# Kernel optimization log

Measured on AMD Instinct MI355X. Metric: run time of the kernel, lower is better.

The kernel has to match this reference:

```python
import jax, jax.numpy as jnp
import numpy as np

PATCH = 14          # config.patch_size
MAX_SEQ = 2048      # config.max_vit_seq_len
A2 = 4              # adaptor_patch_size ** 2
GRID = 32           # max_image_size // patch_size -> sqrt(num_positions - 1)
EPS = 1e-5          # layer_norm_eps

IMG_SIZES = [(448, 448), (448, 672), (336, 336), (224, 448), (560, 560), (336, 448)]


def bilinear_resize_chw(img, oh, ow):
    # torch F.interpolate(mode='bilinear', align_corners=False): half-pixel centers, edge clamp
    C, H, W = img.shape
    def coords(o, i):
        c = (jnp.arange(o, dtype=jnp.float32) + 0.5) * (i / o) - 0.5
        c = jnp.clip(c, 0.0, i - 1.0)
        lo = jnp.floor(c).astype(jnp.int32)
        hi = jnp.minimum(lo + 1, i - 1)
        return lo, hi, c - lo
    y0, y1, wy = coords(oh, H)
    x0, x1, wx = coords(ow, W)
    top = img[:, y0][:, :, x0] * (1 - wx) + img[:, y0][:, :, x1] * wx
    bot = img[:, y1][:, :, x0] * (1 - wx) + img[:, y1][:, :, x1] * wx
    wy = wy[None, :, None]
    return top * (1 - wy) + bot * wy


def patch_embed(img, conv_w, conv_b):
    # Conv2d(k=stride=PATCH) == non-overlapping patch extract + matmul
    C, H, W = img.shape
    h, w = H // PATCH, W // PATCH
    x = img[:, :h * PATCH, :w * PATCH].reshape(C, h, PATCH, w, PATCH)
    x = x.transpose(1, 3, 0, 2, 4).reshape(h * w, C * PATCH * PATCH)  # [hw, c*kh*kw]
    out = x @ conv_w.reshape(conv_w.shape[0], -1).T + conv_b          # [hw, E]
    return out, (h, w)


def pos_embed_interp(pos_table, h, w):
    pe = pos_table[1:]  # drop cls position, [GRID*GRID, E]
    if (h, w) == (GRID, GRID):
        return pe
    E = pe.shape[-1]
    pe2d = pe.reshape(GRID, GRID, E).transpose(2, 0, 1)  # [E, GRID, GRID]
    pe2d = bilinear_resize_chw(pe2d, h, w)
    return pe2d.transpose(1, 2, 0).reshape(h * w, E)


def layernorm(x, g, b):
    m = x.mean(-1, keepdims=True)
    v = ((x - m) ** 2).mean(-1, keepdims=True)
    return (x - m) / jnp.sqrt(v + EPS) * g + b


def pack_positions(hw_list):
    # static replay of group_images_by_max_seq_len + a2 rescale in forward
    pos, batch_idx, seq_len = [], 0, 0
    for (h, w) in hw_list:
        L = h * w
        if seq_len + L > MAX_SEQ:
            batch_idx += 1
            seq_len = 0
        s = (seq_len // A2) * A2
        pos.append((batch_idx, s, s + (L // A2) * A2))
        seq_len += L
    return pos, batch_idx + 1


def setup_inputs() -> dict:
    key = jax.random.key(0)
    ks = jax.random.split(key, 9)
    E = 1280
    inp = {}
    for i, (H, W) in enumerate(IMG_SIZES):
        inp[f'img{i}'] = jax.random.normal(ks[i], (3, H, W), dtype=jnp.float32)
    inp['conv_w'] = jax.random.normal(ks[6], (E, 3, PATCH, PATCH), dtype=jnp.float32) * 0.02
    inp['conv_b'] = jnp.zeros((E,), dtype=jnp.float32)
    inp['pos_table'] = jax.random.normal(ks[7], (GRID * GRID + 1, E), dtype=jnp.float32) * 0.02
    inp['ln_w'] = jnp.ones((E,), dtype=jnp.float32)
    inp['ln_b'] = jnp.zeros((E,), dtype=jnp.float32)
    return inp


def reference(img0, img1, img2, img3, img4, img5, conv_w, conv_b, pos_table, ln_w, ln_b):
    images = [img0, img1, img2, img3, img4, img5]
    E = conv_w.shape[0]
    hw = [(im.shape[1] // PATCH, im.shape[2] // PATCH) for im in images]
    positions, B = pack_positions(hw)
    emb = jnp.zeros((B, MAX_SEQ, E), dtype=jnp.float32)
    mask = np.zeros((B, 1, MAX_SEQ, MAX_SEQ), dtype=bool)
    for im, (bi, s, e) in zip(images, positions):
        x, (h, w) = patch_embed(im, conv_w, conv_b)
        x = x + pos_embed_interp(pos_table, h, w)
        x = layernorm(x, ln_w, ln_b)
        emb = emb.at[bi, s:e].set(x)
        mask[bi, 0, s:e, s:e] = True
    return emb, jnp.asarray(mask)
```

## Files before the change

kernel.cpp:

```cpp
#include <hip/hip_runtime.h>
#include <hip/hip_bf16.h>
#include <stdint.h>

#define E_DIM 1280
#define KDIM 588
#define KPAD 608
#define M_TOTAL 6016
#define EMB_FLOATS (5*2048*1280)
#define MASK_FLOATS (5*2048*2048)

typedef __attribute__((ext_vector_type(8))) short bf16x8;
typedef __attribute__((ext_vector_type(4))) float f32x4;

__device__ __forceinline__ unsigned short f2bf(float f) {
    unsigned int u = __float_as_uint(f);
    u += 0x7fff + ((u >> 16) & 1);
    return (unsigned short)(u >> 16);
}

__global__ __launch_bounds__(256) void extract_patches(
    const float* __restrict__ i0, const float* __restrict__ i1,
    const float* __restrict__ i2, const float* __restrict__ i3,
    const float* __restrict__ i4, const float* __restrict__ i5,
    unsigned short* __restrict__ A)
{
    int idx = blockIdx.x * 256 + threadIdx.x;
    if (idx >= M_TOTAL * KPAD) return;
    int r = idx / KPAD;
    int k = idx - r * KPAD;
    unsigned short v = 0;
    if (k < KDIM) {
        const int rowOff[7] = {0,1024,2560,3136,3648,5248,6016};
        const int wA[6]     = {32,48,24,32,40,32};
        const int WA[6]     = {448,672,336,448,560,448};
        const int planeA[6] = {200704,301056,112896,100352,313600,150528};
        const float* imgs[6] = {i0,i1,i2,i3,i4,i5};
        int img = 0;
        #pragma unroll
        for (int i = 1; i < 6; ++i) if (r >= rowOff[i]) img = i;
        int ri = r - rowOff[img];
        int w = wA[img], W = WA[img], plane = planeA[img];
        int py = ri / w, px = ri - py * w;
        int c  = k / 196;
        int rem = k - c * 196;
        int iy = rem / 14, ix = rem - iy * 14;
        float pix = imgs[img][(size_t)c * plane + (size_t)(py*14 + iy) * W + (px*14 + ix)];
        v = f2bf(pix);
    }
    A[idx] = v;
}

__global__ __launch_bounds__(256) void convert_w(
    const float* __restrict__ cw, unsigned short* __restrict__ Wb)
{
    int idx = blockIdx.x * 256 + threadIdx.x;
    if (idx >= E_DIM * KPAD) return;
    int e = idx / KPAD;
    int k = idx - e * KPAD;
    Wb[idx] = (k < KDIM) ? f2bf(cw[(size_t)e * KDIM + k]) : (unsigned short)0;
}

__global__ __launch_bounds__(256) void gemm_bf16(
    const unsigned short* __restrict__ A,
    const unsigned short* __restrict__ Bm,
    float* __restrict__ C)
{
    __shared__ __align__(16) unsigned short As[128*32];
    __shared__ __align__(16) unsigned short Bs[128*32];
    const int t  = threadIdx.x;
    const int m0 = blockIdx.x * 128;
    const int n0 = blockIdx.y * 128;
    const int lane = t & 63;
    const int wv = t >> 6;
    const int wr = wv >> 1, wc = wv & 1;
    const int l16 = lane & 15, q = lane >> 4;

    f32x4 acc[4][4] = {};

    for (int kk = 0; kk < KPAD; kk += 32) {
        #pragma unroll
        for (int i = 0; i < 2; ++i) {
            int off = i * 4096 + t * 16;
            int row = off >> 6;
            int kb  = (off & 63) >> 1;
            const unsigned short* ga = A  + (size_t)(m0 + row) * KPAD + kk + kb;
            __builtin_amdgcn_global_load_lds(
                (const __attribute__((address_space(1))) void*)ga,
                (__attribute__((address_space(3))) void*)((char*)As + off), 16, 0, 0);
            const unsigned short* gb = Bm + (size_t)(n0 + row) * KPAD + kk + kb;
            __builtin_amdgcn_global_load_lds(
                (const __attribute__((address_space(1))) void*)gb,
                (__attribute__((address_space(3))) void*)((char*)Bs + off), 16, 0, 0);
        }
        __syncthreads();

        bf16x8 af[4], bfr[4];
        #pragma unroll
        for (int mi = 0; mi < 4; ++mi)
            af[mi] = *(const bf16x8*)&As[(wr*64 + mi*16 + l16) * 32 + q * 8];
        #pragma unroll
        for (int ni = 0; ni < 4; ++ni)
            bfr[ni] = *(const bf16x8*)&Bs[(wc*64 + ni*16 + l16) * 32 + q * 8];
        #pragma unroll
        for (int mi = 0; mi < 4; ++mi)
            #pragma unroll
            for (int ni = 0; ni < 4; ++ni)
                acc[mi][ni] = __builtin_amdgcn_mfma_f32_16x16x32_bf16(
                    af[mi], bfr[ni], acc[mi][ni], 0, 0, 0);
        __syncthreads();
    }

    #pragma unroll
    for (int mi = 0; mi < 4; ++mi) {
        #pragma unroll
        for (int ni = 0; ni < 4; ++ni) {
            int col = n0 + wc*64 + ni*16 + l16;
            #pragma unroll
            for (int reg = 0; reg < 4; ++reg) {
                int rowr = m0 + wr*64 + mi*16 + q*4 + reg;
                C[(size_t)rowr * E_DIM + col] = acc[mi][ni][reg];
            }
        }
    }
}

__global__ __launch_bounds__(256) void epilogue(
    const float* __restrict__ C, const float* __restrict__ pos_table,
    const float* __restrict__ conv_b,
    const float* __restrict__ ln_w, const float* __restrict__ ln_b,
    float* __restrict__ out)
{
    const int r = blockIdx.x;
    const int t = threadIdx.x;
    const int rowOff[7]  = {0,1024,2560,3136,3648,5248,6016};
    const int hA[6]      = {32,32,24,16,40,24};
    const int wA[6]      = {32,48,24,32,40,32};
    const int outBase[6] = {0, 2048, 4096, 4672, 6144, 8192};

    int img = 0;
    #pragma unroll
    for (int i = 1; i < 6; ++i) if (r >= rowOff[i]) img = i;
    int ri = r - rowOff[img];
    int h = hA[img], w = wA[img];
    int y = ri / w, x = ri - y * w;

    float cy = fminf(fmaxf((y + 0.5f) * (32.0f / h) - 0.5f, 0.0f), 31.0f);
    float cx = fminf(fmaxf((x + 0.5f) * (32.0f / w) - 0.5f, 0.0f), 31.0f);
    int y0 = (int)floorf(cy); int y1 = min(y0 + 1, 31); float wy = cy - (float)y0;
    int x0 = (int)floorf(cx); int x1 = min(x0 + 1, 31); float wx = cx - (float)x0;

    const float* P00 = pos_table + (size_t)(1 + y0*32 + x0) * E_DIM;
    const float* P01 = pos_table + (size_t)(1 + y0*32 + x1) * E_DIM;
    const float* P10 = pos_table + (size_t)(1 + y1*32 + x0) * E_DIM;
    const float* P11 = pos_table + (size_t)(1 + y1*32 + x1) * E_DIM;

    float vals[5];
    float s = 0.f, s2 = 0.f;
    #pragma unroll
    for (int j = 0; j < 5; ++j) {
        int e = t + j * 256;
        float p = (1.f - wy) * ((1.f - wx) * P00[e] + wx * P01[e])
                +        wy  * ((1.f - wx) * P10[e] + wx * P11[e]);
        float v = C[(size_t)r * E_DIM + e] + conv_b[e] + p;
        vals[j] = v;
        s += v; s2 += v * v;
    }
    #pragma unroll
    for (int o = 32; o > 0; o >>= 1) {
        s  += __shfl_down(s,  o, 64);
        s2 += __shfl_down(s2, o, 64);
    }
    __shared__ float ls[8];
    int lane = t & 63, wvi = t >> 6;
    if (lane == 0) { ls[wvi] = s; ls[4 + wvi] = s2; }
    __syncthreads();
    if (t == 0) {
        float ts  = ls[0] + ls[1] + ls[2] + ls[3];
        float ts2 = ls[4] + ls[5] + ls[6] + ls[7];
        float m   = ts / 1280.f;
        float var = ts2 / 1280.f - m * m;
        ls[0] = m;
        ls[1] = 1.f / sqrtf(var + 1e-5f);
    }
    __syncthreads();
    float m = ls[0], inv = ls[1];
    size_t ob = (size_t)(outBase[img] + ri) * E_DIM;
    #pragma unroll
    for (int j = 0; j < 5; ++j) {
        int e = t + j * 256;
        out[ob + e] = (vals[j] - m) * inv * ln_w[e] + ln_b[e];
    }
}

__global__ __launch_bounds__(256) void fill_rest(float4* __restrict__ out4)
{
    const int TOT4 = (EMB_FLOATS + MASK_FLOATS) / 4;
    int idx = blockIdx.x * 256 + threadIdx.x;
    if (idx >= TOT4) return;
    size_t flat = (size_t)idx * 4;
    if (flat < (size_t)EMB_FLOATS) {
        int row = (int)(flat / E_DIM);
        int b   = row >> 11;
        int seq = row & 2047;
        const int filled[5] = {1024,1536,1088,1600,768};
        if (seq >= filled[b]) {
            out4[idx] = make_float4(0.f, 0.f, 0.f, 0.f);
        }
    } else {
        size_t mrem = flat - (size_t)EMB_FLOATS;
        int b  = (int)(mrem >> 22);
        int rr = (int)(mrem >> 11) & 2047;
        int c0 = (int)(mrem & 2047);
        const int h0[5] = {1024,1536,576,1600,768};
        const int l1[5] = {0,0,576,0,0};
        const int h1[5] = {0,0,1088,0,0};
        bool rin0 = rr < h0[b];
        bool rin1 = (rr >= l1[b]) && (rr < h1[b]) && (h1[b] > 0);
        float4 v;
        float* vp = &v.x;
        #pragma unroll
        for (int j = 0; j < 4; ++j) {
            int c = c0 + j;
            bool on = (rin0 && c < h0[b]) ||
                      (rin1 && c >= l1[b] && c < h1[b]);
            vp[j] = on ? 1.f : 0.f;
        }
        out4[idx] = v;
    }
}

extern "C" void kernel_launch(void* const* d_in, const int* in_sizes, int n_in,
                              void* d_out, int out_size, void* d_ws, size_t ws_size,
                              hipStream_t stream) {
    const float* img0 = (const float*)d_in[0];
    const float* img1 = (const float*)d_in[1];
    const float* img2 = (const float*)d_in[2];
    const float* img3 = (const float*)d_in[3];
    const float* img4 = (const float*)d_in[4];
    const float* img5 = (const float*)d_in[5];
    const float* conv_w    = (const float*)d_in[6];
    const float* conv_b    = (const float*)d_in[7];
    const float* pos_table = (const float*)d_in[8];
    const float* ln_w      = (const float*)d_in[9];
    const float* ln_b      = (const float*)d_in[10];
    float* out = (float*)d_out;

    unsigned short* Abf = (unsigned short*)d_ws;
    unsigned short* Wbf = Abf + (size_t)M_TOTAL * KPAD;
    float* Cbuf = out + EMB_FLOATS;

    int nA = M_TOTAL * KPAD;
    extract_patches<<<(nA + 255) / 256, 256, 0, stream>>>(
        img0, img1, img2, img3, img4, img5, Abf);

    int nW = E_DIM * KPAD;
    convert_w<<<(nW + 255) / 256, 256, 0, stream>>>(conv_w, Wbf);

    dim3 g(M_TOTAL / 128, E_DIM / 128);
    gemm_bf16<<<g, 256, 0, stream>>>(Abf, Wbf, Cbuf);

    epilogue<<<M_TOTAL, 256, 0, stream>>>(Cbuf, pos_table, conv_b, ln_w, ln_b, out);

    int tot4 = (EMB_FLOATS + MASK_FLOATS) / 4;
    fill_rest<<<(tot4 + 255) / 256, 256, 0, stream>>>((float4*)out);
}
```

Before: 219.6 us.

## Fuse prep, weight convert, and fill into one launch; vectorize epilogue

Merges patch extraction, weight bf16 conversion, padding-row zeroing and mask filling into a single kernel. Each image gets its own block range with template-constant dimensions, and only the unfilled embedding rows are zeroed. The GEMM output buffer moves from the mask region to workspace, so mask writes no longer have to wait until after the epilogue. The epilogue uses 320 threads each handling one float4, which cuts per-row memory instructions at the cost of assuming the workspace is large enough for the extra C buffer.

```diff
diff --git a/kernel.cpp b/kernel.cpp
--- a/kernel.cpp
+++ b/kernel.cpp
@@ -9,6 +9,12 @@
 #define EMB_FLOATS (5*2048*1280)
 #define MASK_FLOATS (5*2048*2048)
 
+#define EXT_BLOCKS  14288
+#define CW_BLOCKS   3040
+#define ZERO_BLOCKS 5280
+#define MASK_BLOCKS 20480
+#define TOTAL_BLOCKS (EXT_BLOCKS + CW_BLOCKS + ZERO_BLOCKS + MASK_BLOCKS)
+
 typedef __attribute__((ext_vector_type(8))) short bf16x8;
 typedef __attribute__((ext_vector_type(4))) float f32x4;
 
@@ -18,46 +24,82 @@
     return (unsigned short)(u >> 16);
 }
 
-__global__ __launch_bounds__(256) void extract_patches(
+template<int PW, int IMGW, int PLANE>
+__device__ __forceinline__ void do_extract(const float* __restrict__ img,
+                                           unsigned short* __restrict__ A,
+                                           int flatBase, int local)
+{
+    int r_local = local / KPAD;
+    int k = local - r_local * KPAD;
+    unsigned short v = 0;
+    if (k < KDIM) {
+        int py = r_local / PW;  int px = r_local - py * PW;
+        int c  = k / 196;       int rem = k - c * 196;
+        int iy = rem / 14;      int ix = rem - iy * 14;
+        v = f2bf(img[(size_t)c * PLANE + (size_t)(py*14 + iy) * IMGW + (px*14 + ix)]);
+    }
+    A[flatBase + local] = v;
+}
+
+__global__ __launch_bounds__(256) void fused_prep(
     const float* __restrict__ i0, const float* __restrict__ i1,
     const float* __restrict__ i2, const float* __restrict__ i3,
     const float* __restrict__ i4, const float* __restrict__ i5,
-    unsigned short* __restrict__ A)
-{
-    int idx = blockIdx.x * 256 + threadIdx.x;
-    if (idx >= M_TOTAL * KPAD) return;
-    int r = idx / KPAD;
-    int k = idx - r * KPAD;
-    unsigned short v = 0;
-    if (k < KDIM) {
-        const int rowOff[7] = {0,1024,2560,3136,3648,5248,6016};
-        const int wA[6]     = {32,48,24,32,40,32};
-        const int WA[6]     = {448,672,336,448,560,448};
-        const int planeA[6] = {200704,301056,112896,100352,313600,150528};
-        const float* imgs[6] = {i0,i1,i2,i3,i4,i5};
-        int img = 0;
-        #pragma unroll
-        for (int i = 1; i < 6; ++i) if (r >= rowOff[i]) img = i;
-        int ri = r - rowOff[img];
-        int w = wA[img], W = WA[img], plane = planeA[img];
-        int py = ri / w, px = ri - py * w;
-        int c  = k / 196;
-        int rem = k - c * 196;
-        int iy = rem / 14, ix = rem - iy * 14;
-        float pix = imgs[img][(size_t)c * plane + (size_t)(py*14 + iy) * W + (px*14 + ix)];
-        v = f2bf(pix);
-    }
-    A[idx] = v;
-}
-
-__global__ __launch_bounds__(256) void convert_w(
-    const float* __restrict__ cw, unsigned short* __restrict__ Wb)
-{
-    int idx = blockIdx.x * 256 + threadIdx.x;
-    if (idx >= E_DIM * KPAD) return;
-    int e = idx / KPAD;
-    int k = idx - e * KPAD;
-    Wb[idx] = (k < KDIM) ? f2bf(cw[(size_t)e * KDIM + k]) : (unsigned short)0;
+    const float* __restrict__ conv_w,
+    unsigned short* __restrict__ A, unsigned short* __restrict__ Wb,
+    float4* __restrict__ out4)
+{
+    const int bid = blockIdx.x;
+    const int t = threadIdx.x;
+
+    if (bid < EXT_BLOCKS) {
+        if (bid < 2432) {
+            int local = bid * 256 + t;
+            do_extract<32,448,200704>(i0, A, 0, local);
+        } else if (bid < 6080) {
+            int local = (bid - 2432) * 256 + t;
+            do_extract<48,672,301056>(i1, A, 2432*256, local);
+        } else if (bid < 7448) {
+            int local = (bid - 6080) * 256 + t;
+            do_extract<24,336,112896>(i2, A, 6080*256, local);
+        } else if (bid < 8664) {
+            int local = (bid - 7448) * 256 + t;
+            do_extract<32,448,100352>(i3, A, 7448*256, local);
+        } else if (bid < 12464) {
+            int local = (bid - 8664) * 256 + t;
+            do_extract<40,560,313600>(i4, A, 8664*256, local);
+        } else {
+            int local = (bid - 12464) * 256 + t;
+            do_extract<32,448,150528>(i5, A, 12464*256, local);
+        }
+    } else if (bid < EXT_BLOCKS + CW_BLOCKS) {
+        int idx = (bid - EXT_BLOCKS) * 256 + t;
+        int e = idx / KPAD;
+        int k = idx - e * KPAD;
+        Wb[idx] = (k < KDIM) ? f2bf(conv_w[(size_t)e * KDIM + k]) : (unsigned short)0;
+    } else if (bid < EXT_BLOCKS + CW_BLOCKS + ZERO_BLOCKS) {
+        int idx = (bid - EXT_BLOCKS - CW_BLOCKS) * 256 + t;
+        int zrow = idx / 320;
+        int c4   = idx - zrow * 320;
+        int b, rowInB;
+        if      (zrow < 1024) { b = 0; rowInB = 1024 + zrow; }
+        else if (zrow < 1536) { b = 1; rowInB = 1536 + (zrow - 1024); }
+        else if (zrow < 2496) { b = 2; rowInB = 1088 + (zrow - 1536); }
+        else if (zrow < 2944) { b = 3; rowInB = 1600 + (zrow - 2496); }
+        else                  { b = 4; rowInB =  768 + (zrow - 2944); }
+        size_t o4 = ((size_t)(b * 2048 + rowInB) * E_DIM) / 4 + c4;
+        out4[o4] = make_float4(0.f, 0.f, 0.f, 0.f);
+    } else {
+        int m4 = (bid - EXT_BLOCKS - CW_BLOCKS - ZERO_BLOCKS) * 256 + t;
+        int b  = m4 >> 20;
+        int rr = (m4 >> 9) & 2047;
+        int c0 = (m4 & 511) * 4;
+        int h0 = (b == 0) ? 1024 : (b == 1) ? 1536 : (b == 2) ? 576 : (b == 3) ? 1600 : 768;
+        bool on = (rr < h0 && c0 < h0);
+        if (b == 2) on = on || (rr >= 576 && rr < 1088 && c0 >= 576 && c0 < 1088);
+        float f = on ? 1.f : 0.f;
+        out4[(size_t)(EMB_FLOATS / 4) + m4] = make_float4(f, f, f, f);
+    }
 }
 
 __global__ __launch_bounds__(256) void gemm_bf16(
@@ -124,7 +166,7 @@
     }
 }
 
-__global__ __launch_bounds__(256) void epilogue(
+__global__ __launch_bounds__(320) void epilogue(
     const float* __restrict__ C, const float* __restrict__ pos_table,
     const float* __restrict__ conv_b,
     const float* __restrict__ ln_w, const float* __restrict__ ln_b,
@@ -132,16 +174,14 @@
 {
     const int r = blockIdx.x;
     const int t = threadIdx.x;
-    const int rowOff[7]  = {0,1024,2560,3136,3648,5248,6016};
-    const int hA[6]      = {32,32,24,16,40,24};
-    const int wA[6]      = {32,48,24,32,40,32};
-    const int outBase[6] = {0, 2048, 4096, 4672, 6144, 8192};
-
-    int img = 0;
-    #pragma unroll
-    for (int i = 1; i < 6; ++i) if (r >= rowOff[i]) img = i;
-    int ri = r - rowOff[img];
-    int h = hA[img], w = wA[img];
+
+    int img     = (r < 1024) ? 0 : (r < 2560) ? 1 : (r < 3136) ? 2 : (r < 3648) ? 3 : (r < 5248) ? 4 : 5;
+    int rowOff  = (img == 0) ? 0 : (img == 1) ? 1024 : (img == 2) ? 2560 : (img == 3) ? 3136 : (img == 4) ? 3648 : 5248;
+    int h       = (img == 0) ? 32 : (img == 1) ? 32 : (img == 2) ? 24 : (img == 3) ? 16 : (img == 4) ? 40 : 24;
+    int w       = (img == 0) ? 32 : (img == 1) ? 48 : (img == 2) ? 24 : (img == 3) ? 32 : (img == 4) ? 40 : 32;
+    int outBase = (img == 0) ? 0 : (img == 1) ? 2048 : (img == 2) ? 4096 : (img == 3) ? 4672 : (img == 4) ? 6144 : 8192;
+
+    int ri = r - rowOff;
     int y = ri / w, x = ri - y * w;
 
     float cy = fminf(fmaxf((y + 0.5f) * (32.0f / h) - 0.5f, 0.0f), 31.0f);
@@ -149,34 +189,38 @@
     int y0 = (int)floorf(cy); int y1 = min(y0 + 1, 31); float wy = cy - (float)y0;
     int x0 = (int)floorf(cx); int x1 = min(x0 + 1, 31); float wx = cx - (float)x0;
 
-    const float* P00 = pos_table + (size_t)(1 + y0*32 + x0) * E_DIM;
-    const float* P01 = pos_table + (size_t)(1 + y0*32 + x1) * E_DIM;
-    const float* P10 = pos_table + (size_t)(1 + y1*32 + x0) * E_DIM;
-    const float* P11 = pos_table + (size_t)(1 + y1*32 + x1) * E_DIM;
-
-    float vals[5];
-    float s = 0.f, s2 = 0.f;
-    #pragma unroll
-    for (int j = 0; j < 5; ++j) {
-        int e = t + j * 256;
-        float p = (1.f - wy) * ((1.f - wx) * P00[e] + wx * P01[e])
-                +        wy  * ((1.f - wx) * P10[e] + wx * P11[e]);
-        float v = C[(size_t)r * E_DIM + e] + conv_b[e] + p;
-        vals[j] = v;
-        s += v; s2 += v * v;
-    }
+    const float4* P00 = (const float4*)(pos_table + (size_t)(1 + y0*32 + x0) * E_DIM);
+    const float4* P01 = (const float4*)(pos_table + (size_t)(1 + y0*32 + x1) * E_DIM);
+    const float4* P10 = (const float4*)(pos_table + (size_t)(1 + y1*32 + x0) * E_DIM);
+    const float4* P11 = (const float4*)(pos_table + (size_t)(1 + y1*32 + x1) * E_DIM);
+    const float4* C4  = (const float4*)(C + (size_t)r * E_DIM);
+    const float4* B4  = (const float4*)conv_b;
+
+    float w00 = (1.f - wy) * (1.f - wx), w01 = (1.f - wy) * wx;
+    float w10 = wy * (1.f - wx),         w11 = wy * wx;
+
+    float4 a = P00[t], b2 = P01[t], c2 = P10[t], d2 = P11[t];
+    float4 cv = C4[t], bv = B4[t];
+    float4 v;
+    v.x = cv.x + bv.x + w00*a.x + w01*b2.x + w10*c2.x + w11*d2.x;
+    v.y = cv.y + bv.y + w00*a.y + w01*b2.y + w10*c2.y + w11*d2.y;
+    v.z = cv.z + bv.z + w00*a.z + w01*b2.z + w10*c2.z + w11*d2.z;
+    v.w = cv.w + bv.w + w00*a.w + w01*b2.w + w10*c2.w + w11*d2.w;
+
+    float s  = v.x + v.y + v.z + v.w;
+    float s2 = v.x*v.x + v.y*v.y + v.z*v.z + v.w*v.w;
     #pragma unroll
     for (int o = 32; o > 0; o >>= 1) {
         s  += __shfl_down(s,  o, 64);
         s2 += __shfl_down(s2, o, 64);
     }
-    __shared__ float ls[8];
+    __shared__ float ls[12];
     int lane = t & 63, wvi = t >> 6;
-    if (lane == 0) { ls[wvi] = s; ls[4 + wvi] = s2; }
+    if (lane == 0) { ls[wvi] = s; ls[6 + wvi] = s2; }
     __syncthreads();
     if (t == 0) {
-        float ts  = ls[0] + ls[1] + ls[2] + ls[3];
-        float ts2 = ls[4] + ls[5] + ls[6] + ls[7];
+        float ts  = ls[0] + ls[1] + ls[2] + ls[3] + ls[4];
+        float ts2 = ls[6] + ls[7] + ls[8] + ls[9] + ls[10];
         float m   = ts / 1280.f;
         float var = ts2 / 1280.f - m * m;
         ls[0] = m;
@@ -184,49 +228,14 @@
     }
     __syncthreads();
     float m = ls[0], inv = ls[1];
-    size_t ob = (size_t)(outBase[img] + ri) * E_DIM;
-    #pragma unroll
-    for (int j = 0; j < 5; ++j) {
-        int e = t + j * 256;
-        out[ob + e] = (vals[j] - m) * inv * ln_w[e] + ln_b[e];
-    }
-}
-
-__global__ __launch_bounds__(256) void fill_rest(float4* __restrict__ out4)
-{
-    const int TOT4 = (EMB_FLOATS + MASK_FLOATS) / 4;
-    int idx = blockIdx.x * 256 + threadIdx.x;
-    if (idx >= TOT4) return;
-    size_t flat = (size_t)idx * 4;
-    if (flat < (size_t)EMB_FLOATS) {
-        int row = (int)(flat / E_DIM);
-        int b   = row >> 11;
-        int seq = row & 2047;
-        const int filled[5] = {1024,1536,1088,1600,768};
-        if (seq >= filled[b]) {
-            out4[idx] = make_float4(0.f, 0.f, 0.f, 0.f);
-        }
-    } else {
-        size_t mrem = flat - (size_t)EMB_FLOATS;
-        int b  = (int)(mrem >> 22);
-        int rr = (int)(mrem >> 11) & 2047;
-        int c0 = (int)(mrem & 2047);
-        const int h0[5] = {1024,1536,576,1600,768};
-        const int l1[5] = {0,0,576,0,0};
-        const int h1[5] = {0,0,1088,0,0};
-        bool rin0 = rr < h0[b];
-        bool rin1 = (rr >= l1[b]) && (rr < h1[b]) && (h1[b] > 0);
-        float4 v;
-        float* vp = &v.x;
-        #pragma unroll
-        for (int j = 0; j < 4; ++j) {
-            int c = c0 + j;
-            bool on = (rin0 && c < h0[b]) ||
-                      (rin1 && c >= l1[b] && c < h1[b]);
-            vp[j] = on ? 1.f : 0.f;
-        }
-        out4[idx] = v;
-    }
+
+    float4 g = ((const float4*)ln_w)[t], be = ((const float4*)ln_b)[t];
+    float4 o4;
+    o4.x = (v.x - m) * inv * g.x + be.x;
+    o4.y = (v.y - m) * inv * g.y + be.y;
+    o4.z = (v.z - m) * inv * g.z + be.z;
+    o4.w = (v.w - m) * inv * g.w + be.w;
+    ((float4*)(out + (size_t)(outBase + ri) * E_DIM))[t] = o4;
 }
 
 extern "C" void kernel_launch(void* const* d_in, const int* in_sizes, int n_in,
@@ -247,20 +256,13 @@
 
     unsigned short* Abf = (unsigned short*)d_ws;
     unsigned short* Wbf = Abf + (size_t)M_TOTAL * KPAD;
-    float* Cbuf = out + EMB_FLOATS;
-
-    int nA = M_TOTAL * KPAD;
-    extract_patches<<<(nA + 255) / 256, 256, 0, stream>>>(
-        img0, img1, img2, img3, img4, img5, Abf);
-
-    int nW = E_DIM * KPAD;
-    convert_w<<<(nW + 255) / 256, 256, 0, stream>>>(conv_w, Wbf);
+    float* Cbuf = (float*)(Wbf + (size_t)E_DIM * KPAD);
+
+    fused_prep<<<TOTAL_BLOCKS, 256, 0, stream>>>(
+        img0, img1, img2, img3, img4, img5, conv_w, Abf, Wbf, (float4*)out);
 
     dim3 g(M_TOTAL / 128, E_DIM / 128);
     gemm_bf16<<<g, 256, 0, stream>>>(Abf, Wbf, Cbuf);
 
-    epilogue<<<M_TOTAL, 256, 0, stream>>>(Cbuf, pos_table, conv_b, ln_w, ln_b, out);
-
-    int tot4 = (EMB_FLOATS + MASK_FLOATS) / 4;
-    fill_rest<<<(tot4 + 255) / 256, 256, 0, stream>>>((float4*)out);
-}
+    epilogue<<<M_TOTAL, 320, 0, stream>>>(Cbuf, pos_table, conv_b, ln_w, ln_b, out);
+}
```

Result: faster. 210.0 us (-4.4%).
